# Performance work log

Hardware: AMD Instinct MI355X
Metric: run time of the kernel (lower is better)

## Reference

```python
import jax, jax.numpy as jnp
import numpy as np

B, S, D = 8, 2048, 768
DK = 768
OUT = 10
EPS = 1e-5

def _layernorm(x, w, b):
    mu = jnp.mean(x, axis=-1, keepdims=True)
    var = jnp.mean(jnp.square(x - mu), axis=-1, keepdims=True)
    return (x - mu) * jax.lax.rsqrt(var + EPS) * w + b

def setup_inputs() -> dict:
    key = jax.random.key(0)
    ks = jax.random.split(key, 8)
    sc_in = 1.0 / np.sqrt(D)
    sc_k = 1.0 / np.sqrt(DK)
    return {
        "src": jax.random.normal(ks[0], (B, S, D), dtype=jnp.float32),
        # weights stored as [in, out] so y = x @ W (equivalent to torch x @ W.T)
        "Wq": jax.random.uniform(ks[1], (D, DK), jnp.float32, -sc_in, sc_in),
        "Wk": jax.random.uniform(ks[2], (D, DK), jnp.float32, -sc_in, sc_in),
        "Wv": jax.random.uniform(ks[3], (D, DK), jnp.float32, -sc_in, sc_in),
        "Wo": jax.random.uniform(ks[4], (DK, D), jnp.float32, -sc_k, sc_k),
        "bo": jnp.zeros((D,), jnp.float32),
        "ln1_w": jnp.ones((D,), jnp.float32),
        "ln1_b": jnp.zeros((D,), jnp.float32),
        "ln2_w": jnp.ones((D,), jnp.float32),
        "ln2_b": jnp.zeros((D,), jnp.float32),
        "Wc": jax.random.uniform(ks[5], (D, OUT), jnp.float32, -sc_in, sc_in),
        "bc": jnp.zeros((OUT,), jnp.float32),
    }

def reference(src, Wq, Wk, Wv, Wo, bo, ln1_w, ln1_b, ln2_w, ln2_b, Wc, bc):
    # Attention (dropout in eval mode -> identity)
    Q = src @ Wq  # [B,S,DK]
    K = src @ Wk
    V = src @ Wv
    scores = jnp.einsum('bsd,btd->bst', Q, K) * (DK ** -0.5)
    attn = jax.nn.softmax(scores, axis=-1)
    out = jnp.einsum('bst,btd->bsd', attn, V) @ Wo + bo
    x = src + out
    x = _layernorm(x, ln1_w, ln1_b)
    x = _layernorm(x, ln2_w, ln2_b)
    pooled = jnp.mean(x, axis=1)  # [B,D]
    logits = pooled @ Wc + bc     # [B,OUT]
    return (logits, x)
```

## Files before the change

kernel.cpp:

```cpp
#include <hip/hip_runtime.h>
#include <cmath>

typedef unsigned short ushort_t;
typedef __bf16 bf16x8 __attribute__((ext_vector_type(8)));
typedef float  f32x4  __attribute__((ext_vector_type(4)));

#define B_  8
#define S_  2048
#define D_  768
#define MROWS (B_ * S_)
#define EPS 1e-5f
#define LDST 40

__device__ __forceinline__ float b2f(ushort_t u) {
    union { unsigned int i; float f; } v; v.i = ((unsigned int)u) << 16; return v.f;
}
__device__ __forceinline__ ushort_t f2b(float f) {
    union { float f; unsigned int i; } v; v.f = f;
    unsigned int r = v.i + 0x7fffu + ((v.i >> 16) & 1u);
    return (ushort_t)(r >> 16);
}

__device__ __forceinline__ void gload16(const ushort_t* g, ushort_t* l) {
    __builtin_amdgcn_global_load_lds((__attribute__((address_space(1))) void*)g,
                                     (__attribute__((address_space(3))) void*)l,
                                     16, 0, 0);
}

__global__ void cast_f32_bf16(const float* __restrict__ in, ushort_t* __restrict__ outp, long n)
{
    const long i = ((long)blockIdx.x * 256 + threadIdx.x) * 4;
    if (i + 3 < n) {
        const float4 v = *(const float4*)(in + i);
        ushort4 o;
        o.x = f2b(v.x); o.y = f2b(v.y); o.z = f2b(v.z); o.w = f2b(v.w);
        *(ushort4*)(outp + i) = o;
    }
}

template<int F32IN>
__global__ void transpose_any(const void* __restrict__ srcv, ushort_t* __restrict__ dst,
                              int R, int C, long sb, long db)
{
    __shared__ ushort_t tile[64 * 65];
    dst += (long)blockIdx.z * db;
    const int r0 = blockIdx.y * 64, c0 = blockIdx.x * 64;
    const int t = threadIdx.x;
    const int tr = t >> 6, tc = t & 63;
    #pragma unroll
    for (int i = 0; i < 16; i++) {
        const int r = i * 4 + tr;
        ushort_t v;
        if (F32IN) v = f2b(((const float*)srcv + (long)blockIdx.z * sb)[(long)(r0 + r) * C + (c0 + tc)]);
        else       v = ((const ushort_t*)srcv + (long)blockIdx.z * sb)[(long)(r0 + r) * C + (c0 + tc)];
        tile[r * 65 + tc] = v;
    }
    __syncthreads();
    #pragma unroll
    for (int i = 0; i < 16; i++) {
        const int r = i * 4 + tr;
        dst[(long)(c0 + r) * R + (r0 + tc)] = tile[tc * 65 + r];
    }
}

template<int MODE>
__global__ __launch_bounds__(256)
void gemm_nt(const ushort_t* __restrict__ A, const ushort_t* __restrict__ Bt,
             void* __restrict__ Cv, int M, int N, int Kd,
             long batchA, long batchB, long batchC, float scale,
             const float* __restrict__ bias, const float* __restrict__ resid)
{
    __shared__ __align__(16) ushort_t As[128 * 32];
    __shared__ __align__(16) ushort_t Bs[128 * 32];

    const int bz = blockIdx.z;
    A  += (long)bz * batchA;
    Bt += (long)bz * batchB;

    const int nxt  = gridDim.x;
    const int nblk = nxt * gridDim.y;
    int lin = blockIdx.y * nxt + blockIdx.x;
    if ((nblk & 7) == 0) {
        const int per = nblk >> 3;
        lin = (lin & 7) * per + (lin >> 3);
    }
    const int tile_n = (lin % nxt) * 128;
    const int tile_m = (lin / nxt) * 128;

    const int tid  = threadIdx.x;
    const int w    = tid >> 6;
    const int lane = tid & 63;
    const int wr = w >> 1, wc = w & 1;
    const int r16 = lane & 15;
    const int kq  = lane >> 4;

    const int srow   = lane >> 2;
    const int schunk = lane & 3;
    const int arow0 = w * 32 + srow;
    const int arow1 = arow0 + 16;
    const int g0 = (schunk ^ ((arow0 >> 1) & 3)) * 8;
    const int g1 = (schunk ^ ((arow1 >> 1) & 3)) * 8;

    const ushort_t* Ar0 = A  + (long)(tile_m + arow0) * Kd + g0;
    const ushort_t* Ar1 = A  + (long)(tile_m + arow1) * Kd + g1;
    const ushort_t* Br0 = Bt + (long)(tile_n + arow0) * Kd + g0;
    const ushort_t* Br1 = Bt + (long)(tile_n + arow1) * Kd + g1;

    ushort_t* lA0 = &As[(w * 32     ) * 32];
    ushort_t* lA1 = &As[(w * 32 + 16) * 32];
    ushort_t* lB0 = &Bs[(w * 32     ) * 32];
    ushort_t* lB1 = &Bs[(w * 32 + 16) * 32];

    f32x4 acc[4][4] = {};

    for (int k0 = 0; k0 < Kd; k0 += 32) {
        gload16(Ar0 + k0, lA0);
        gload16(Ar1 + k0, lA1);
        gload16(Br0 + k0, lB0);
        gload16(Br1 + k0, lB1);
        __syncthreads();

        bf16x8 af[4], bg[4];
        #pragma unroll
        for (int i = 0; i < 4; i++) {
            const int ra = wr * 64 + i * 16 + r16;
            af[i] = *reinterpret_cast<const bf16x8*>(&As[ra * 32 + ((kq ^ ((ra >> 1) & 3)) * 8)]);
            const int rb = wc * 64 + i * 16 + r16;
            bg[i] = *reinterpret_cast<const bf16x8*>(&Bs[rb * 32 + ((kq ^ ((rb >> 1) & 3)) * 8)]);
        }
        #pragma unroll
        for (int mi = 0; mi < 4; mi++)
            #pragma unroll
            for (int ni = 0; ni < 4; ni++)
                acc[mi][ni] = __builtin_amdgcn_mfma_f32_16x16x32_bf16(af[mi], bg[ni], acc[mi][ni], 0, 0, 0);
        __syncthreads();
    }

    if (MODE == 0) {
        ushort_t* C = (ushort_t*)Cv + (long)bz * batchC;
        #pragma unroll
        for (int mi = 0; mi < 4; mi++)
            #pragma unroll
            for (int ni = 0; ni < 4; ni++)
                #pragma unroll
                for (int r = 0; r < 4; r++) {
                    const int row = tile_m + wr * 64 + mi * 16 + kq * 4 + r;
                    const int col = tile_n + wc * 64 + ni * 16 + r16;
                    C[(long)row * N + col] = f2b(acc[mi][ni][r] * scale);
                }
    } else {
        float* C = (float*)Cv;
        #pragma unroll
        for (int mi = 0; mi < 4; mi++)
            #pragma unroll
            for (int ni = 0; ni < 4; ni++)
                #pragma unroll
                for (int r = 0; r < 4; r++) {
                    const int row = tile_m + wr * 64 + mi * 16 + kq * 4 + r;
                    const int col = tile_n + wc * 64 + ni * 16 + r16;
                    C[(long)row * N + col] =
                        acc[mi][ni][r] + bias[col] + resid[(long)row * N + col];
                }
    }
}

template<int TRANSB, int MODE, int BF32>
__global__ __launch_bounds__(256)
void gemm_s(const ushort_t* __restrict__ A, const void* __restrict__ Bsrc,
            void* __restrict__ Cv, int M, int N, int Kd, float scale,
            const float* __restrict__ bias, const float* __restrict__ resid)
{
    __shared__ __align__(16) ushort_t As[128 * LDST];
    __shared__ __align__(16) ushort_t Bs[128 * LDST];
    const int tile_n = blockIdx.x * 128;
    const int tile_m = blockIdx.y * 128;
    const int tid  = threadIdx.x;
    const int w    = tid >> 6;
    const int lane = tid & 63;
    const int wr = w >> 1, wc = w & 1;
    const int r16 = lane & 15;
    const int kq  = lane >> 4;
    f32x4 acc[4][4] = {};
    for (int k0 = 0; k0 < Kd; k0 += 32) {
        #pragma unroll
        for (int cc = 0; cc < 2; cc++) {
            const int c = tid + cc * 256;
            const int row = c >> 2, col = (c & 3) * 8;
            *(uint4*)&As[row * LDST + col] = *(const uint4*)(A + (long)(tile_m + row) * Kd + k0 + col);
        }
        if (TRANSB == 0) {
            const ushort_t* Bt = (const ushort_t*)Bsrc;
            #pragma unroll
            for (int cc = 0; cc < 2; cc++) {
                const int c = tid + cc * 256;
                const int row = c >> 2, col = (c & 3) * 8;
                *(uint4*)&Bs[row * LDST + col] = *(const uint4*)(Bt + (long)(tile_n + row) * Kd + k0 + col);
            }
        } else {
            #pragma unroll
            for (int i = 0; i < 16; i++) {
                const int lin = i * 256 + tid;
                const int kr = lin >> 7, nc = lin & 127;
                ushort_t bv;
                if (BF32) bv = f2b(((const float*)Bsrc)[(long)(k0 + kr) * N + tile_n + nc]);
                else      bv = ((const ushort_t*)Bsrc)[(long)(k0 + kr) * N + tile_n + nc];
                Bs[nc * LDST + kr] = bv;
            }
        }
        __syncthreads();
        bf16x8 af[4], bg[4];
        #pragma unroll
        for (int i = 0; i < 4; i++) {
            af[i] = *reinterpret_cast<const bf16x8*>(&As[(wr * 64 + i * 16 + r16) * LDST + kq * 8]);
            bg[i] = *reinterpret_cast<const bf16x8*>(&Bs[(wc * 64 + i * 16 + r16) * LDST + kq * 8]);
        }
        #pragma unroll
        for (int mi = 0; mi < 4; mi++)
            #pragma unroll
            for (int ni = 0; ni < 4; ni++)
                acc[mi][ni] = __builtin_amdgcn_mfma_f32_16x16x32_bf16(af[mi], bg[ni], acc[mi][ni], 0, 0, 0);
        __syncthreads();
    }
    if (MODE == 0) {
        ushort_t* C = (ushort_t*)Cv;
        #pragma unroll
        for (int mi = 0; mi < 4; mi++)
            #pragma unroll
            for (int ni = 0; ni < 4; ni++)
                #pragma unroll
                for (int r = 0; r < 4; r++) {
                    const int row = tile_m + wr * 64 + mi * 16 + kq * 4 + r;
                    const int col = tile_n + wc * 64 + ni * 16 + r16;
                    C[(long)row * N + col] = f2b(acc[mi][ni][r] * scale);
                }
    } else {
        float* C = (float*)Cv;
        #pragma unroll
        for (int mi = 0; mi < 4; mi++)
            #pragma unroll
            for (int ni = 0; ni < 4; ni++)
                #pragma unroll
                for (int r = 0; r < 4; r++) {
                    const int row = tile_m + wr * 64 + mi * 16 + kq * 4 + r;
                    const int col = tile_n + wc * 64 + ni * 16 + r16;
                    C[(long)row * N + col] =
                        acc[mi][ni][r] + bias[col] + resid[(long)row * N + col];
                }
    }
}

__global__ void softmax_rows(ushort_t* __restrict__ p)
{
    __shared__ float sm[4], ss_[4];
    ushort_t* pr = p + (long)blockIdx.x * 2048;
    const int tid = threadIdx.x;
    const int w = tid >> 6;
    const uint4 raw = *(const uint4*)(pr + tid * 8);
    float v[8];
    v[0] = b2f((ushort_t)(raw.x & 0xffff)); v[1] = b2f((ushort_t)(raw.x >> 16));
    v[2] = b2f((ushort_t)(raw.y & 0xffff)); v[3] = b2f((ushort_t)(raw.y >> 16));
    v[4] = b2f((ushort_t)(raw.z & 0xffff)); v[5] = b2f((ushort_t)(raw.z >> 16));
    v[6] = b2f((ushort_t)(raw.w & 0xffff)); v[7] = b2f((ushort_t)(raw.w >> 16));
    float mx = -3.0e38f;
    #pragma unroll
    for (int i = 0; i < 8; i++) mx = fmaxf(mx, v[i]);
    #pragma unroll
    for (int off = 32; off; off >>= 1) mx = fmaxf(mx, __shfl_xor(mx, off));
    if ((tid & 63) == 0) sm[w] = mx;
    __syncthreads();
    mx = fmaxf(fmaxf(sm[0], sm[1]), fmaxf(sm[2], sm[3]));
    float s = 0.f;
    #pragma unroll
    for (int i = 0; i < 8; i++) { v[i] = __expf(v[i] - mx); s += v[i]; }
    #pragma unroll
    for (int off = 32; off; off >>= 1) s += __shfl_xor(s, off);
    if ((tid & 63) == 0) ss_[w] = s;
    __syncthreads();
    s = ss_[0] + ss_[1] + ss_[2] + ss_[3];
    const float inv = 1.f / s;
    uint4 o;
    o.x = f2b(v[0] * inv) | ((unsigned)f2b(v[1] * inv) << 16);
    o.y = f2b(v[2] * inv) | ((unsigned)f2b(v[3] * inv) << 16);
    o.z = f2b(v[4] * inv) | ((unsigned)f2b(v[5] * inv) << 16);
    o.w = f2b(v[6] * inv) | ((unsigned)f2b(v[7] * inv) << 16);
    *(uint4*)(pr + tid * 8) = o;
}

__global__ void ln_fused(float* __restrict__ x,
                         const float* __restrict__ w1, const float* __restrict__ b1,
                         const float* __restrict__ w2, const float* __restrict__ b2)
{
    __shared__ float r1s[4], r1q[4], r2s[4], r2q[4];
    const long row = blockIdx.x;
    const int tid = threadIdx.x;
    const int w = tid >> 6;
    float* xr = x + row * 768;
    float v[3], s = 0.f, q = 0.f;
    #pragma unroll
    for (int i = 0; i < 3; i++) { const float t = xr[tid + i * 256]; v[i] = t; s += t; q += t * t; }
    #pragma unroll
    for (int off = 32; off; off >>= 1) { s += __shfl_xor(s, off); q += __shfl_xor(q, off); }
    if ((tid & 63) == 0) { r1s[w] = s; r1q[w] = q; }
    __syncthreads();
    s = r1s[0] + r1s[1] + r1s[2] + r1s[3];
    q = r1q[0] + r1q[1] + r1q[2] + r1q[3];
    float mu = s * (1.f / 768.f);
    float ri = rsqrtf(q * (1.f / 768.f) - mu * mu + EPS);
    float y[3];
    s = 0.f; q = 0.f;
    #pragma unroll
    for (int i = 0; i < 3; i++) {
        const int d = tid + i * 256;
        const float t = (v[i] - mu) * ri * w1[d] + b1[d];
        y[i] = t; s += t; q += t * t;
    }
    #pragma unroll
    for (int off = 32; off; off >>= 1) { s += __shfl_xor(s, off); q += __shfl_xor(q, off); }
    if ((tid & 63) == 0) { r2s[w] = s; r2q[w] = q; }
    __syncthreads();
    s = r2s[0] + r2s[1] + r2s[2] + r2s[3];
    q = r2q[0] + r2q[1] + r2q[2] + r2q[3];
    mu = s * (1.f / 768.f);
    ri = rsqrtf(q * (1.f / 768.f) - mu * mu + EPS);
    #pragma unroll
    for (int i = 0; i < 3; i++) {
        const int d = tid + i * 256;
        xr[d] = (y[i] - mu) * ri * w2[d] + b2[d];
    }
}

__global__ void pool_reduce(const float* __restrict__ x, float* __restrict__ pooled)
{
    const int d  = blockIdx.x * 256 + threadIdx.x;
    const int b  = blockIdx.z;
    const int sp = blockIdx.y;
    const float* base = x + ((long)b * 2048 + sp * 128) * 768 + d;
    float s = 0.f;
    #pragma unroll 8
    for (int i = 0; i < 128; i++) s += base[(long)i * 768];
    atomicAdd(&pooled[b * 768 + d], s);
}

__global__ void logits_kernel(const float* __restrict__ pooled, const float* __restrict__ Wc,
                              const float* __restrict__ bc, float* __restrict__ out)
{
    const int t = threadIdx.x;
    if (t < 80) {
        const int b = t / 10, o = t % 10;
        const float* pb = pooled + b * 768;
        float s = bc[o];
        for (int d = 0; d < 768; d++) s += pb[d] * (1.f / 2048.f) * Wc[d * 10 + o];
        out[b * 10 + o] = s;
    }
}

extern "C" void kernel_launch(void* const* d_in, const int* in_sizes, int n_in,
                              void* d_out, int out_size, void* d_ws, size_t ws_size,
                              hipStream_t stream)
{
    (void)in_sizes; (void)n_in; (void)out_size;
    const float* src  = (const float*)d_in[0];
    const float* Wq   = (const float*)d_in[1];
    const float* Wk   = (const float*)d_in[2];
    const float* Wv   = (const float*)d_in[3];
    const float* Wo   = (const float*)d_in[4];
    const float* bo   = (const float*)d_in[5];
    const float* ln1w = (const float*)d_in[6];
    const float* ln1b = (const float*)d_in[7];
    const float* ln2w = (const float*)d_in[8];
    const float* ln2b = (const float*)d_in[9];
    const float* Wc   = (const float*)d_in[10];
    const float* bc   = (const float*)d_in[11];
    float* out = (float*)d_out;

    const dim3 blk(256);
    const float qscale = 1.0f / sqrtf(768.0f);
    const long bs = (long)2048 * 768;

    const size_t WT    = (size_t)768 * 768 * 2;
    const size_t BUF   = (size_t)MROWS * 768 * 2;
    const size_t POOLB = 24576;
    const size_t PROBS8 = (size_t)8 * 2048 * 2048 * 2;
    const size_t needB = 4 * WT + 5 * BUF + POOLB;
    const size_t needA = needB + PROBS8;

    char* ws = (char*)d_ws;
    size_t off = 0;
    auto alloc = [&](size_t bytes) { void* p = ws + off; off += (bytes + 255) & ~(size_t)255; return p; };

    if (ws_size >= needB) {
        ushort_t* Wtq  = (ushort_t*)alloc(WT);
        ushort_t* Wtk  = (ushort_t*)alloc(WT);
        ushort_t* Wtv  = (ushort_t*)alloc(WT);
        ushort_t* Wto  = (ushort_t*)alloc(WT);
        ushort_t* srcb = (ushort_t*)alloc(BUF);
        ushort_t* Qb   = (ushort_t*)alloc(BUF);
        ushort_t* Kb   = (ushort_t*)alloc(BUF);
        ushort_t* Vb   = (ushort_t*)alloc(BUF);
        ushort_t* Vt   = (ushort_t*)alloc(BUF);
        float*  pooled = (float*)  alloc(POOLB);
        const bool batched = (ws_size >= needA);
        ushort_t* probs = batched ? (ushort_t*)alloc(PROBS8) : srcb;
        ushort_t* attn  = Vb;
        float*    xpre  = out + 80;

        cast_f32_bf16<<<MROWS * 768 / 1024, blk, 0, stream>>>(src, srcb, (long)MROWS * 768);
        transpose_any<1><<<dim3(12, 12, 1), blk, 0, stream>>>(Wq, Wtq, 768, 768, 0, 0);
        transpose_any<1><<<dim3(12, 12, 1), blk, 0, stream>>>(Wk, Wtk, 768, 768, 0, 0);
        transpose_any<1><<<dim3(12, 12, 1), blk, 0, stream>>>(Wv, Wtv, 768, 768, 0, 0);
        transpose_any<1><<<dim3(12, 12, 1), blk, 0, stream>>>(Wo, Wto, 768, 768, 0, 0);

        gemm_nt<0><<<dim3(6, 128, 1), blk, 0, stream>>>(srcb, Wtq, Qb, MROWS, 768, 768, 0, 0, 0, qscale, nullptr, nullptr);
        gemm_nt<0><<<dim3(6, 128, 1), blk, 0, stream>>>(srcb, Wtk, Kb, MROWS, 768, 768, 0, 0, 0, 1.0f, nullptr, nullptr);
        gemm_nt<0><<<dim3(6, 128, 1), blk, 0, stream>>>(srcb, Wtv, Vb, MROWS, 768, 768, 0, 0, 0, 1.0f, nullptr, nullptr);

        transpose_any<0><<<dim3(12, 32, B_), blk, 0, stream>>>(Vb, Vt, 2048, 768, bs, bs);

        if (batched) {
            gemm_nt<0><<<dim3(16, 16, B_), blk, 0, stream>>>(Qb, Kb, probs, 2048, 2048, 768,
                                                             bs, bs, (long)2048 * 2048, 1.0f, nullptr, nullptr);
            softmax_rows<<<B_ * 2048, blk, 0, stream>>>(probs);
            gemm_nt<0><<<dim3(6, 16, B_), blk, 0, stream>>>(probs, Vt, attn, 2048, 768, 2048,
                                                            (long)2048 * 2048, bs, bs, 1.0f, nullptr, nullptr);
        } else {
            for (int bz = 0; bz < B_; bz += 2) {
                gemm_nt<0><<<dim3(16, 16, 2), blk, 0, stream>>>(Qb + bz * bs, Kb + bz * bs, probs,
                                                                2048, 2048, 768, bs, bs, (long)2048 * 2048,
                                                                1.0f, nullptr, nullptr);
                softmax_rows<<<2 * 2048, blk, 0, stream>>>(probs);
                gemm_nt<0><<<dim3(6, 16, 2), blk, 0, stream>>>(probs, Vt, attn + bz * bs, 2048, 768, 2048,
                                                               (long)2048 * 2048, bs, bs, 1.0f, nullptr, nullptr);
            }
        }

        gemm_nt<1><<<dim3(6, 128, 1), blk, 0, stream>>>(attn, Wto, xpre, MROWS, 768, 768, 0, 0, 0, 1.0f, bo, src);
        ln_fused<<<MROWS, blk, 0, stream>>>(xpre, ln1w, ln1b, ln2w, ln2b);
        hipMemsetAsync(pooled, 0, B_ * 768 * 4, stream);
        pool_reduce<<<dim3(3, 16, B_), blk, 0, stream>>>(xpre, pooled);
        logits_kernel<<<1, 128, 0, stream>>>(pooled, Wc, bc, out);
    } else {
        ushort_t* srcb = (ushort_t*)alloc(BUF);
        ushort_t* Qb   = (ushort_t*)alloc(BUF);
        ushort_t* Kb   = (ushort_t*)alloc(BUF);
        ushort_t* Vb   = (ushort_t*)alloc(BUF);
        float*  pooled = (float*)  alloc(POOLB);
        ushort_t* probs = srcb;
        ushort_t* attn  = Qb;
        float*    xpre  = out + 80;

        cast_f32_bf16<<<MROWS * 768 / 1024, blk, 0, stream>>>(src, srcb, (long)MROWS * 768);
        gemm_s<1, 0, 1><<<dim3(6, 128), blk, 0, stream>>>(srcb, Wq, Qb, MROWS, 768, 768, qscale, nullptr, nullptr);
        gemm_s<1, 0, 1><<<dim3(6, 128), blk, 0, stream>>>(srcb, Wk, Kb, MROWS, 768, 768, 1.0f, nullptr, nullptr);
        gemm_s<1, 0, 1><<<dim3(6, 128), blk, 0, stream>>>(srcb, Wv, Vb, MROWS, 768, 768, 1.0f, nullptr, nullptr);
        for (int bz = 0; bz < B_; bz++) {
            gemm_s<0, 0, 0><<<dim3(16, 16), blk, 0, stream>>>(Qb + bz * bs, Kb + bz * bs, probs,
                                                              2048, 2048, 768, 1.0f, nullptr, nullptr);
            softmax_rows<<<2048, blk, 0, stream>>>(probs);
            gemm_s<1, 0, 0><<<dim3(6, 16), blk, 0, stream>>>(probs, Vb + bz * bs, attn + bz * bs,
                                                             2048, 768, 2048, 1.0f, nullptr, nullptr);
        }
        gemm_s<1, 1, 1><<<dim3(6, 128), blk, 0, stream>>>(attn, Wo, xpre, MROWS, 768, 768, 1.0f, bo, src);
        ln_fused<<<MROWS, blk, 0, stream>>>(xpre, ln1w, ln1b, ln2w, ln2b);
        hipMemsetAsync(pooled, 0, B_ * 768 * 4, stream);
        pool_reduce<<<dim3(3, 16, B_), blk, 0, stream>>>(xpre, pooled);
        logits_kernel<<<1, 128, 0, stream>>>(pooled, Wc, bc, out);
    }
}
```

Before: 521.1 us.

## Fuse softmax into QK^T and PV GEMM epilogues, merge QKV projections

The QK^T GEMM epilogue now writes exp(score) directly and accumulates row sums with shuffles and atomics. The PV GEMM epilogue divides by those row sums, so the separate softmax pass over the full probability matrix is gone. The three Q/K/V projections run as one GEMM over the contiguous transposed weights, writing into the contiguous Q/K/V buffers, and the logits kernel is parallelised across 80 blocks. Dropping the max subtraction risks overflow if scores grow large, and the atomics add contention on row sums.

```diff
diff --git a/kernel.cpp b/kernel.cpp
--- a/kernel.cpp
+++ b/kernel.cpp
@@ -68,7 +68,8 @@
 void gemm_nt(const ushort_t* __restrict__ A, const ushort_t* __restrict__ Bt,
              void* __restrict__ Cv, int M, int N, int Kd,
              long batchA, long batchB, long batchC, float scale,
-             const float* __restrict__ bias, const float* __restrict__ resid)
+             const float* __restrict__ bias, const float* __restrict__ resid,
+             float* __restrict__ rowsum)
 {
     __shared__ __align__(16) ushort_t As[128 * 32];
     __shared__ __align__(16) ushort_t Bs[128 * 32];
@@ -148,7 +149,7 @@
                     const int col = tile_n + wc * 64 + ni * 16 + r16;
                     C[(long)row * N + col] = f2b(acc[mi][ni][r] * scale);
                 }
-    } else {
+    } else if (MODE == 1) {
         float* C = (float*)Cv;
         #pragma unroll
         for (int mi = 0; mi < 4; mi++)
@@ -160,6 +161,61 @@
                     const int col = tile_n + wc * 64 + ni * 16 + r16;
                     C[(long)row * N + col] =
                         acc[mi][ni][r] + bias[col] + resid[(long)row * N + col];
+                }
+    } else if (MODE == 2) {
+        ushort_t* C = (ushort_t*)Cv + (long)bz * batchC;
+        const float* rs = rowsum + (long)bz * 2048;
+        #pragma unroll
+        for (int mi = 0; mi < 4; mi++) {
+            float inv[4];
+            #pragma unroll
+            for (int r = 0; r < 4; r++)
+                inv[r] = 1.0f / rs[tile_m + wr * 64 + mi * 16 + kq * 4 + r];
+            #pragma unroll
+            for (int ni = 0; ni < 4; ni++)
+                #pragma unroll
+                for (int r = 0; r < 4; r++) {
+                    const int row = tile_m + wr * 64 + mi * 16 + kq * 4 + r;
+                    const int col = tile_n + wc * 64 + ni * 16 + r16;
+                    C[(long)row * N + col] = f2b(acc[mi][ni][r] * inv[r]);
+                }
+        }
+    } else if (MODE == 3) {
+        ushort_t* C = (ushort_t*)Cv + (long)bz * batchC;
+        float* rs = rowsum + (long)bz * 2048;
+        #pragma unroll
+        for (int mi = 0; mi < 4; mi++)
+            #pragma unroll
+            for (int r = 0; r < 4; r++) {
+                const int row = tile_m + wr * 64 + mi * 16 + kq * 4 + r;
+                float psum = 0.f;
+                #pragma unroll
+                for (int ni = 0; ni < 4; ni++) {
+                    const float e = __expf(acc[mi][ni][r] * scale);
+                    psum += e;
+                    const int col = tile_n + wc * 64 + ni * 16 + r16;
+                    C[(long)row * N + col] = f2b(e);
+                }
+                psum += __shfl_xor(psum, 1);
+                psum += __shfl_xor(psum, 2);
+                psum += __shfl_xor(psum, 4);
+                psum += __shfl_xor(psum, 8);
+                if (r16 == 0) atomicAdd(&rs[row], psum);
+            }
+    } else {
+        const int sect  = tile_n / 768;
+        const int ncol0 = tile_n - sect * 768;
+        ushort_t* C = (ushort_t*)Cv + (size_t)sect * ((size_t)MROWS * 768);
+        const float sc = (sect == 0) ? scale : 1.0f;
+        #pragma unroll
+        for (int mi = 0; mi < 4; mi++)
+            #pragma unroll
+            for (int ni = 0; ni < 4; ni++)
+                #pragma unroll
+                for (int r = 0; r < 4; r++) {
+                    const int row = tile_m + wr * 64 + mi * 16 + kq * 4 + r;
+                    const int col = ncol0 + wc * 64 + ni * 16 + r16;
+                    C[(long)row * 768 + col] = f2b(acc[mi][ni][r] * sc);
                 }
     }
 }
@@ -344,14 +400,14 @@
 __global__ void logits_kernel(const float* __restrict__ pooled, const float* __restrict__ Wc,
                               const float* __restrict__ bc, float* __restrict__ out)
 {
-    const int t = threadIdx.x;
-    if (t < 80) {
-        const int b = t / 10, o = t % 10;
-        const float* pb = pooled + b * 768;
-        float s = bc[o];
-        for (int d = 0; d < 768; d++) s += pb[d] * (1.f / 2048.f) * Wc[d * 10 + o];
-        out[b * 10 + o] = s;
-    }
+    const int b = blockIdx.x / 10, o = blockIdx.x % 10;
+    const int lane = threadIdx.x;
+    float s = 0.f;
+    #pragma unroll
+    for (int d = lane; d < 768; d += 64) s += pooled[b * 768 + d] * Wc[d * 10 + o];
+    #pragma unroll
+    for (int off = 32; off; off >>= 1) s += __shfl_xor(s, off);
+    if (lane == 0) out[b * 10 + o] = s * (1.f / 2048.f) + bc[o];
 }
 
 extern "C" void kernel_launch(void* const* d_in, const int* in_sizes, int n_in,
@@ -380,8 +436,9 @@
     const size_t WT    = (size_t)768 * 768 * 2;
     const size_t BUF   = (size_t)MROWS * 768 * 2;
     const size_t POOLB = 24576;
+    const size_t RSB   = (size_t)B_ * 2048 * 4;
     const size_t PROBS8 = (size_t)8 * 2048 * 2048 * 2;
-    const size_t needB = 4 * WT + 5 * BUF + POOLB;
+    const size_t needB = 4 * WT + 5 * BUF + POOLB + RSB;
     const size_t needA = needB + PROBS8;
 
     char* ws = (char*)d_ws;
@@ -399,6 +456,7 @@
         ushort_t* Vb   = (ushort_t*)alloc(BUF);
         ushort_t* Vt   = (ushort_t*)alloc(BUF);
         float*  pooled = (float*)  alloc(POOLB);
+        float*  rowsum = (float*)  alloc(RSB);
         const bool batched = (ws_size >= needA);
         ushort_t* probs = batched ? (ushort_t*)alloc(PROBS8) : srcb;
         ushort_t* attn  = Vb;
@@ -410,34 +468,37 @@
         transpose_any<1><<<dim3(12, 12, 1), blk, 0, stream>>>(Wv, Wtv, 768, 768, 0, 0);
         transpose_any<1><<<dim3(12, 12, 1), blk, 0, stream>>>(Wo, Wto, 768, 768, 0, 0);
 
-        gemm_nt<0><<<dim3(6, 128, 1), blk, 0, stream>>>(srcb, Wtq, Qb, MROWS, 768, 768, 0, 0, 0, qscale, nullptr, nullptr);
-        gemm_nt<0><<<dim3(6, 128, 1), blk, 0, stream>>>(srcb, Wtk, Kb, MROWS, 768, 768, 0, 0, 0, 1.0f, nullptr, nullptr);
-        gemm_nt<0><<<dim3(6, 128, 1), blk, 0, stream>>>(srcb, Wtv, Vb, MROWS, 768, 768, 0, 0, 0, 1.0f, nullptr, nullptr);
+        gemm_nt<4><<<dim3(18, 128, 1), blk, 0, stream>>>(srcb, Wtq, Qb, MROWS, 2304, 768,
+                                                         0, 0, 0, qscale, nullptr, nullptr, nullptr);
 
         transpose_any<0><<<dim3(12, 32, B_), blk, 0, stream>>>(Vb, Vt, 2048, 768, bs, bs);
+        hipMemsetAsync(rowsum, 0, RSB, stream);
 
         if (batched) {
-            gemm_nt<0><<<dim3(16, 16, B_), blk, 0, stream>>>(Qb, Kb, probs, 2048, 2048, 768,
-                                                             bs, bs, (long)2048 * 2048, 1.0f, nullptr, nullptr);
-            softmax_rows<<<B_ * 2048, blk, 0, stream>>>(probs);
-            gemm_nt<0><<<dim3(6, 16, B_), blk, 0, stream>>>(probs, Vt, attn, 2048, 768, 2048,
-                                                            (long)2048 * 2048, bs, bs, 1.0f, nullptr, nullptr);
+            gemm_nt<3><<<dim3(16, 16, B_), blk, 0, stream>>>(Qb, Kb, probs, 2048, 2048, 768,
+                                                             bs, bs, (long)2048 * 2048, 1.0f,
+                                                             nullptr, nullptr, rowsum);
+            gemm_nt<2><<<dim3(6, 16, B_), blk, 0, stream>>>(probs, Vt, attn, 2048, 768, 2048,
+                                                            (long)2048 * 2048, bs, bs, 1.0f,
+                                                            nullptr, nullptr, rowsum);
         } else {
             for (int bz = 0; bz < B_; bz += 2) {
-                gemm_nt<0><<<dim3(16, 16, 2), blk, 0, stream>>>(Qb + bz * bs, Kb + bz * bs, probs,
+                gemm_nt<3><<<dim3(16, 16, 2), blk, 0, stream>>>(Qb + bz * bs, Kb + bz * bs, probs,
                                                                 2048, 2048, 768, bs, bs, (long)2048 * 2048,
-                                                                1.0f, nullptr, nullptr);
-                softmax_rows<<<2 * 2048, blk, 0, stream>>>(probs);
-                gemm_nt<0><<<dim3(6, 16, 2), blk, 0, stream>>>(probs, Vt, attn + bz * bs, 2048, 768, 2048,
-                                                               (long)2048 * 2048, bs, bs, 1.0f, nullptr, nullptr);
+                                                                1.0f, nullptr, nullptr, rowsum + bz * 2048);
+                gemm_nt<2><<<dim3(6, 16, 2), blk, 0, stream>>>(probs, Vt + bz * bs, attn + bz * bs,
+                                                               2048, 768, 2048,
+                                                               (long)2048 * 2048, bs, bs, 1.0f,
+                                                               nullptr, nullptr, rowsum + bz * 2048);
             }
         }
 
-        gemm_nt<1><<<dim3(6, 128, 1), blk, 0, stream>>>(attn, Wto, xpre, MROWS, 768, 768, 0, 0, 0, 1.0f, bo, src);
+        gemm_nt<1><<<dim3(6, 128, 1), blk, 0, stream>>>(attn, Wto, xpre, MROWS, 768, 768,
+                                                        0, 0, 0, 1.0f, bo, src, nullptr);
         ln_fused<<<MROWS, blk, 0, stream>>>(xpre, ln1w, ln1b, ln2w, ln2b);
         hipMemsetAsync(pooled, 0, B_ * 768 * 4, stream);
         pool_reduce<<<dim3(3, 16, B_), blk, 0, stream>>>(xpre, pooled);
-        logits_kernel<<<1, 128, 0, stream>>>(pooled, Wc, bc, out);
+        logits_kernel<<<80, 64, 0, stream>>>(pooled, Wc, bc, out);
     } else {
         ushort_t* srcb = (ushort_t*)alloc(BUF);
         ushort_t* Qb   = (ushort_t*)alloc(BUF);
@@ -463,6 +524,6 @@
         ln_fused<<<MROWS, blk, 0, stream>>>(xpre, ln1w, ln1b, ln2w, ln2b);
         hipMemsetAsync(pooled, 0, B_ * 768 * 4, stream);
         pool_reduce<<<dim3(3, 16, B_), blk, 0, stream>>>(xpre, pooled);
-        logits_kernel<<<1, 128, 0, stream>>>(pooled, Wc, bc, out);
-    }
-}
+        logits_kernel<<<80, 64, 0, stream>>>(pooled, Wc, bc, out);
+    }
+}
```

Result: faster. 474.4 us (-9.0%).
